# Performance work log

Hardware: AMD Instinct MI355X
Metric: run time of the kernel (lower is better)

## Reference

```python
import jax, jax.numpy as jnp
import numpy as np

B, S, D = 2, 2048, 2048
H, G = 32, 8           # num_heads, num_groups
HD = D // H            # head_dim = 64
GS = H // G            # group_size = 4


def setup_inputs() -> dict:
    key = jax.random.key(0)
    ks = jax.random.split(key, 11)
    s = 0.02
    return {
        "x": jax.random.normal(ks[0], (B, S, D), dtype=jnp.float32),
        "kv": jax.random.normal(ks[1], (B, S, D), dtype=jnp.float32),
        "Wq": jax.random.normal(ks[2], (D, D), dtype=jnp.float32) * s,
        "bq": jnp.zeros((D,), dtype=jnp.float32),
        "Wk": jax.random.normal(ks[3], (D, G * HD), dtype=jnp.float32) * s,
        "bk": jnp.zeros((G * HD,), dtype=jnp.float32),
        "Wv": jax.random.normal(ks[4], (D, G * HD), dtype=jnp.float32) * s,
        "bv": jnp.zeros((G * HD,), dtype=jnp.float32),
        "Wo": jax.random.normal(ks[5], (D, D), dtype=jnp.float32) * s,
        "bo": jnp.zeros((D,), dtype=jnp.float32),
        "expanding_context": 0,
    }


def reference(x, kv, Wq, bq, Wk, bk, Wv, bv, Wo, bo, expanding_context):
    # expanding_context is ignored when use_kv_cache=False (matches torch module)
    b, s, d = x.shape
    q = (x @ Wq + bq).reshape(b, s, H, HD).transpose(0, 2, 1, 3)      # [B,H,S,HD]
    k = (kv @ Wk + bk).reshape(b, s, G, HD).transpose(0, 2, 1, 3)     # [B,G,S,HD]
    v = (kv @ Wv + bv).reshape(b, s, G, HD).transpose(0, 2, 1, 3)     # [B,G,S,HD]
    # repeat_interleave KV heads to match query heads
    k = jnp.repeat(k, GS, axis=1)                                      # [B,H,S,HD]
    v = jnp.repeat(v, GS, axis=1)
    scale = 1.0 / jnp.sqrt(jnp.array(HD, dtype=x.dtype))
    scores = jnp.einsum("bhqd,bhkd->bhqk", q, k) * scale              # [B,H,S,S]
    causal = jnp.tril(jnp.ones((s, s), dtype=bool))                    # True where allowed
    scores = jnp.where(causal[None, None], scores, jnp.finfo(x.dtype).min)
    attn = jax.nn.softmax(scores, axis=-1)
    out = jnp.einsum("bhqk,bhkd->bhqd", attn, v)                      # [B,H,S,HD]
    out = out.transpose(0, 2, 1, 3).reshape(b, s, D)                  # [B,S,D]
    return out @ Wo + bo
```

## Files before the change

kernel.cpp:

```cpp
#include <hip/hip_runtime.h>
#include <hip/hip_bf16.h>
#include <stdint.h>

namespace {
constexpr int CB = 2, CS = 2048, CD = 2048, CH = 32, CG = 8, CHD = 64, CGS = 4;

typedef __bf16 bf16x8 __attribute__((ext_vector_type(8)));
typedef float f32x4 __attribute__((ext_vector_type(4)));
typedef float f32x16 __attribute__((ext_vector_type(16)));
typedef uint32_t u32x4 __attribute__((ext_vector_type(4)));

__device__ inline uint16_t f2bf(float f) {
  uint32_t u = __float_as_uint(f);
  u += 0x7fffu + ((u >> 16) & 1u);
  return (uint16_t)(u >> 16);
}

__device__ inline void gload_lds16(const void* g, void* l) {
  __builtin_amdgcn_global_load_lds(
      (const __attribute__((address_space(1))) void*)g,
      (__attribute__((address_space(3))) void*)l, 16, 0, 0);
}

__device__ inline uint32_t cvtpk_bf16(float lo, float hi) {
  uint32_t r;
  asm("v_cvt_pk_bf16_f32 %0, %1, %2" : "=v"(r) : "v"(lo), "v"(hi));
  return r;
}
__device__ inline void pl32swap(uint32_t& a, uint32_t& b) {
  asm("v_permlane32_swap_b32 %0, %1" : "+v"(a), "+v"(b));
}
}

__global__ __launch_bounds__(256) void cast_both_kernel(
    const float* __restrict__ x, const float* __restrict__ kv,
    uint16_t* __restrict__ xb, uint16_t* __restrict__ kvb, int nel) {
  int i = (blockIdx.x * 256 + threadIdx.x) * 4;
  const float* in;
  uint16_t* out;
  if (i < nel) { in = x + i; out = xb + i; }
  else         { in = kv + (i - nel); out = kvb + (i - nel); }
  const float4 v = *(const float4*)in;
  ushort4 o;
  o.x = f2bf(v.x); o.y = f2bf(v.y); o.z = f2bf(v.z); o.w = f2bf(v.w);
  *(ushort4*)out = o;
}

__global__ __launch_bounds__(256) void transpose_all_kernel(
    const float* __restrict__ Wq, const float* __restrict__ Wk,
    const float* __restrict__ Wv, const float* __restrict__ Wo,
    uint16_t* __restrict__ out) {
  __shared__ uint16_t tile[32][33];
  const int gn0 = blockIdx.x * 32;
  const int k0 = blockIdx.y * 32;
  const float* in;
  int Nr, start;
  if (gn0 < 2048)      { in = Wq; Nr = 2048; start = 0; }
  else if (gn0 < 2560) { in = Wk; Nr = 512;  start = 2048; }
  else if (gn0 < 3072) { in = Wv; Nr = 512;  start = 2560; }
  else                 { in = Wo; Nr = 2048; start = 3072; }
  const int n0 = gn0 - start;
  const int tx = threadIdx.x & 31, tg = threadIdx.x >> 5;
#pragma unroll
  for (int rr = 0; rr < 4; ++rr) {
    int k = tg * 4 + rr;
    tile[k][tx] = f2bf(in[(size_t)(k0 + k) * Nr + n0 + tx]);
  }
  __syncthreads();
#pragma unroll
  for (int rr = 0; rr < 4; ++rr) {
    int n = tg * 4 + rr;
    out[(size_t)(gn0 + n) * CD + k0 + tx] = tile[tx][n];
  }
}

__global__ __launch_bounds__(512, 2) void gemm_qkv_kernel(
    const uint16_t* __restrict__ xb, const uint16_t* __restrict__ kvb,
    const uint16_t* __restrict__ WT,
    const float* __restrict__ bq, const float* __restrict__ bk,
    const float* __restrict__ bv,
    uint16_t* __restrict__ Qb, uint16_t* __restrict__ Kb,
    uint16_t* __restrict__ VTb) {
  constexpr int BM = 256, BN = 256, BK = 64, K = 2048;
  __shared__ uint16_t Asm[2][BM * BK];
  __shared__ uint16_t Bsm[2][BN * BK];
  const int tid = threadIdx.x;
  const int w = tid >> 6, l = tid & 63;
  const int wr = w >> 2, wc = w & 3;
  const int l15 = l & 15, lq = l >> 4;

  const int gx = gridDim.x;
  int bid = blockIdx.y * gx + blockIdx.x;
  const int nwg = gx * gridDim.y;
  bid = (bid & 7) * (nwg >> 3) + (bid >> 3);
  const int m0 = (bid / gx) * BM, n0 = (bid % gx) * BN;
  const uint16_t* A = (n0 < 2048) ? xb : kvb;

  auto stage = [&](int buf, int kt) {
#pragma unroll
    for (int i = 0; i < 4; ++i) {
      int g = i * 512 + tid;
      int row = g >> 3, slot = g & 7;
      int kq = slot ^ (row & 7);
      gload_lds16(A + (size_t)(m0 + row) * K + kt + kq * 8, &Asm[buf][g * 8]);
    }
#pragma unroll
    for (int i = 0; i < 4; ++i) {
      int g = i * 512 + tid;
      int row = g >> 3, slot = g & 7;
      int kq = slot ^ (row & 7);
      gload_lds16(WT + (size_t)(n0 + row) * K + kt + kq * 8, &Bsm[buf][g * 8]);
    }
  };

  f32x4 acc[8][4] = {};

  stage(0, 0);
  asm volatile("s_waitcnt vmcnt(0)" ::: "memory");
  __syncthreads();
  int cur = 0;

  for (int kt = 0; kt < K; kt += BK) {
    if (kt + BK < K) stage(cur ^ 1, kt + BK);

    const char* Ab = (const char*)&Asm[cur][0];
    const char* Bb = (const char*)&Bsm[cur][0];
#pragma unroll
    for (int kk = 0; kk < 2; ++kk) {
      bf16x8 af[8], bfr[4];
#pragma unroll
      for (int m = 0; m < 8; ++m) {
        int row = wr * 128 + m * 16 + l15;
        int boff = ((row * BK + kk * 32 + lq * 8) * 2) ^ ((row & 7) << 4);
        af[m] = *(const bf16x8*)(Ab + boff);
      }
#pragma unroll
      for (int n = 0; n < 4; ++n) {
        int row = wc * 64 + n * 16 + l15;
        int boff = ((row * BK + kk * 32 + lq * 8) * 2) ^ ((row & 7) << 4);
        bfr[n] = *(const bf16x8*)(Bb + boff);
      }
#pragma unroll
      for (int m = 0; m < 8; ++m)
#pragma unroll
        for (int n = 0; n < 4; ++n)
          acc[m][n] = __builtin_amdgcn_mfma_f32_16x16x32_bf16(
              af[m], bfr[n], acc[m][n], 0, 0, 0);
    }

    asm volatile("s_waitcnt vmcnt(0)" ::: "memory");
    __syncthreads();
    cur ^= 1;
  }

#pragma unroll
  for (int m = 0; m < 8; ++m)
#pragma unroll
    for (int n = 0; n < 4; ++n)
#pragma unroll
      for (int r = 0; r < 4; ++r) {
        int gm = m0 + wr * 128 + m * 16 + lq * 4 + r;
        int gn = n0 + wc * 64 + n * 16 + l15;
        int b = gm >> 11, s = gm & (CS - 1);
        if (n0 < 2048) {
          float v = (acc[m][n][r] + bq[gn]) * (0.125f * 1.44269504088896340736f);
          int h = gn >> 6, hd = gn & 63;
          Qb[(((size_t)(b * CH + h)) * CS + s) * CHD + hd] = f2bf(v);
        } else if (n0 < 2560) {
          int gn2 = gn - 2048;
          float v = acc[m][n][r] + bk[gn2];
          int gh = gn2 >> 6, hd = gn2 & 63;
          Kb[(((size_t)(b * CG + gh)) * CS + s) * CHD + hd] = f2bf(v);
        } else {
          int gn2 = gn - 2560;
          float v = acc[m][n][r] + bv[gn2];
          int gh = gn2 >> 6, hd = gn2 & 63;
          VTb[(((size_t)(b * CG + gh)) * CHD + hd) * CS + s] = f2bf(v);
        }
      }
}

__global__ __launch_bounds__(512, 2) void gemm_out_kernel(
    const uint16_t* __restrict__ A, const uint16_t* __restrict__ Bt,
    const float* __restrict__ bias, float* __restrict__ Cout,
    int M, int N, int K) {
  constexpr int BM = 256, BN = 128, BK = 64;
  __shared__ uint16_t Asm[2][BM * BK];
  __shared__ uint16_t Bsm[2][BN * BK];
  const int tid = threadIdx.x;
  const int w = tid >> 6, l = tid & 63;
  const int wr = w >> 2, wc = w & 3;
  const int l15 = l & 15, lq = l >> 4;

  const int gx = gridDim.x;
  int bid = blockIdx.y * gx + blockIdx.x;
  const int nwg = gx * gridDim.y;
  bid = (bid & 7) * (nwg >> 3) + (bid >> 3);
  const int m0 = (bid / gx) * BM, n0 = (bid % gx) * BN;

  auto stage = [&](int buf, int kt) {
#pragma unroll
    for (int i = 0; i < 4; ++i) {
      int g = i * 512 + tid;
      int row = g >> 3, slot = g & 7;
      int kq = slot ^ (row & 7);
      gload_lds16(A + (size_t)(m0 + row) * K + kt + kq * 8, &Asm[buf][g * 8]);
    }
#pragma unroll
    for (int i = 0; i < 2; ++i) {
      int g = i * 512 + tid;
      int row = g >> 3, slot = g & 7;
      int kq = slot ^ (row & 7);
      gload_lds16(Bt + (size_t)(n0 + row) * K + kt + kq * 8, &Bsm[buf][g * 8]);
    }
  };

  f32x4 acc[8][2] = {};

  stage(0, 0);
  asm volatile("s_waitcnt vmcnt(0)" ::: "memory");
  __syncthreads();
  int cur = 0;

  for (int kt = 0; kt < K; kt += BK) {
    if (kt + BK < K) stage(cur ^ 1, kt + BK);

    const char* Ab = (const char*)&Asm[cur][0];
    const char* Bb = (const char*)&Bsm[cur][0];
#pragma unroll
    for (int kk = 0; kk < 2; ++kk) {
      bf16x8 af[8], bfr[2];
#pragma unroll
      for (int m = 0; m < 8; ++m) {
        int row = wr * 128 + m * 16 + l15;
        int boff = ((row * BK + kk * 32 + lq * 8) * 2) ^ ((row & 7) << 4);
        af[m] = *(const bf16x8*)(Ab + boff);
      }
#pragma unroll
      for (int n = 0; n < 2; ++n) {
        int row = wc * 32 + n * 16 + l15;
        int boff = ((row * BK + kk * 32 + lq * 8) * 2) ^ ((row & 7) << 4);
        bfr[n] = *(const bf16x8*)(Bb + boff);
      }
#pragma unroll
      for (int m = 0; m < 8; ++m)
#pragma unroll
        for (int n = 0; n < 2; ++n)
          acc[m][n] = __builtin_amdgcn_mfma_f32_16x16x32_bf16(
              af[m], bfr[n], acc[m][n], 0, 0, 0);
    }

    asm volatile("s_waitcnt vmcnt(0)" ::: "memory");
    __syncthreads();
    cur ^= 1;
  }

#pragma unroll
  for (int m = 0; m < 8; ++m)
#pragma unroll
    for (int n = 0; n < 2; ++n)
#pragma unroll
      for (int r = 0; r < 4; ++r) {
        int gm = m0 + wr * 128 + m * 16 + lq * 4 + r;
        int gn = n0 + wc * 32 + n * 16 + l15;
        Cout[(size_t)gm * N + gn] = acc[m][n][r] + bias[gn];
      }
}

__global__ __launch_bounds__(256) void flash_attn_kernel(
    const uint16_t* __restrict__ Q, const uint16_t* __restrict__ K,
    const uint16_t* __restrict__ VT, uint16_t* __restrict__ Aout) {
  constexpr int NQB = CS / 128;
  __shared__ __align__(16) uint16_t Ksm[2][64 * 64];
  __shared__ __align__(16) uint16_t Vsm[2][64 * 64];
  const int tid = threadIdx.x, w = tid >> 6, l = tid & 63;
  const int l31 = l & 31, hi = l >> 5;
  const int x = blockIdx.x;
  const int h = blockIdx.y, b = blockIdx.z, g = h >> 2;

  const uint16_t* Qbase = Q + ((size_t)(b * CH + h)) * CS * CHD;
  const uint16_t* Kbase = K + ((size_t)(b * CG + g)) * CS * CHD;
  const uint16_t* Vbase = VT + ((size_t)(b * CG + g)) * CHD * CS;

  const int srow = tid >> 3, sslot = tid & 7;
  const int skq = sslot ^ (srow & 7);
  const uint16_t* kSrc0 = Kbase + (size_t)srow * CHD + skq * 8;
  const uint16_t* kSrc1 = kSrc0 + 32 * CHD;
  const uint16_t* vSrc0 = Vbase + (size_t)srow * CS + skq * 8;
  const uint16_t* vSrc1 = vSrc0 + 32 * CS;
  uint16_t* kDst0 = &Ksm[0][0] + tid * 8;
  uint16_t* vDst0 = &Vsm[0][0] + tid * 8;

  int qkOff[2][4];
#pragma unroll
  for (int c = 0; c < 2; ++c)
#pragma unroll
    for (int kc = 0; kc < 4; ++kc) {
      int row = c * 32 + l31;
      qkOff[c][kc] = ((row * 64 + kc * 16 + hi * 8) * 2) ^ ((row & 7) << 4);
    }

  auto stage = [&](int buf, int kt) {
    const size_t ko = (size_t)kt * 64 * CHD;
    const int vo = kt * 64;
    uint16_t* kd = kDst0 + buf * 64 * 64;
    uint16_t* vd = vDst0 + buf * 64 * 64;
    gload_lds16(kSrc0 + ko, kd);
    gload_lds16(kSrc1 + ko, kd + 2048);
    gload_lds16(vSrc0 + vo, vd);
    gload_lds16(vSrc1 + vo, vd + 2048);
  };

#pragma unroll 1
  for (int job = 0; job < 2; ++job) {
    const int qb = job == 0 ? (NQB - 1 - x) : x;
    const int qrow = qb * 128 + w * 32 + l31;
    const int wtop = qb * 128 + w * 32 + 31;

    bf16x8 qf[4];
#pragma unroll
    for (int kc = 0; kc < 4; ++kc)
      qf[kc] = *(const bf16x8*)(Qbase + (size_t)qrow * CHD + kc * 16 + hi * 8);

    f32x16 o0 = {}, o1 = {};
    float mrun = -3e38f, lrun = 0.f;
    const int nt = 2 * qb + 2;

    stage(0, 0);
    asm volatile("s_waitcnt vmcnt(0)" ::: "memory");
    __syncthreads();

    for (int kt = 0; kt < nt; ++kt) {
      const int cur = kt & 1;
      if (kt + 1 < nt) stage(cur ^ 1, kt + 1);

      if (kt * 64 <= wtop) {
        const char* ksmb = (const char*)Ksm[cur];
        const char* vsmb = (const char*)Vsm[cur];

        f32x16 p0 = {}, p1 = {};
        __builtin_amdgcn_s_setprio(1);
#pragma unroll
        for (int kc = 0; kc < 4; ++kc) {
          bf16x8 ka0 = *(const bf16x8*)(ksmb + qkOff[0][kc]);
          bf16x8 ka1 = *(const bf16x8*)(ksmb + qkOff[1][kc]);
          p0 = __builtin_amdgcn_mfma_f32_32x32x16_bf16(ka0, qf[kc], p0, 0, 0, 0);
          p1 = __builtin_amdgcn_mfma_f32_32x32x16_bf16(ka1, qf[kc], p1, 0, 0, 0);
        }
        __builtin_amdgcn_s_setprio(0);

        const bool need_mask = (kt * 64 + 63 > qb * 128 + w * 32);
        float pmax = -3e38f;
        if (need_mask) {
#pragma unroll
          for (int r = 0; r < 16; ++r) {
            int keyb = kt * 64 + (r & 3) + 8 * (r >> 2) + 4 * hi;
            if (keyb > qrow) p0[r] = -3e38f;
            if (keyb + 32 > qrow) p1[r] = -3e38f;
          }
        }
#pragma unroll
        for (int r = 0; r < 16; ++r) {
          pmax = fmaxf(pmax, p0[r]);
          pmax = fmaxf(pmax, p1[r]);
        }
        pmax = fmaxf(pmax, __shfl_xor(pmax, 32));

        if (!__all(pmax <= mrun + 8.f)) {
          float mnew = fmaxf(mrun, pmax);
          float alpha = __builtin_amdgcn_exp2f(mrun - mnew);
#pragma unroll
          for (int r = 0; r < 16; ++r) { o0[r] *= alpha; o1[r] *= alpha; }
          lrun *= alpha;
          mrun = mnew;
        }
        float s = 0.f;
#pragma unroll
        for (int r = 0; r < 16; ++r) {
          float e0 = __builtin_amdgcn_exp2f(p0[r] - mrun);
          float e1 = __builtin_amdgcn_exp2f(p1[r] - mrun);
          p0[r] = e0; p1[r] = e1;
          s += e0 + e1;
        }
        s += __shfl_xor(s, 32);
        lrun += s;

        u32x4 paw[4];
#pragma unroll
        for (int k = 0; k < 4; ++k) {
          const int base = (k & 1) * 8;
          const f32x16& pc = (k >> 1) ? p1 : p0;
          uint32_t c01 = cvtpk_bf16(pc[base + 0], pc[base + 1]);
          uint32_t c23 = cvtpk_bf16(pc[base + 2], pc[base + 3]);
          uint32_t c45 = cvtpk_bf16(pc[base + 4], pc[base + 5]);
          uint32_t c67 = cvtpk_bf16(pc[base + 6], pc[base + 7]);
          pl32swap(c01, c45);
          pl32swap(c23, c67);
          paw[k] = (u32x4){c01, c23, c45, c67};
        }

        __builtin_amdgcn_s_setprio(1);
#pragma unroll
        for (int ks = 0; ks < 4; ++ks) {
          bf16x8 vb0 = *(const bf16x8*)(vsmb + qkOff[0][ks]);
          bf16x8 vb1 = *(const bf16x8*)(vsmb + qkOff[1][ks]);
          bf16x8 pb = __builtin_bit_cast(bf16x8, paw[ks]);
          o0 = __builtin_amdgcn_mfma_f32_32x32x16_bf16(vb0, pb, o0, 0, 0, 0);
          o1 = __builtin_amdgcn_mfma_f32_32x32x16_bf16(vb1, pb, o1, 0, 0, 0);
        }
        __builtin_amdgcn_s_setprio(0);
      }

      asm volatile("s_waitcnt vmcnt(0)" ::: "memory");
      __syncthreads();
    }

    float invl = 1.f / lrun;
    uint16_t* orow = Aout + ((size_t)b * CS + qrow) * CD + (size_t)h * CHD;
#pragma unroll
    for (int k = 0; k < 8; ++k) {
      int reg = 2 * k;
      int hd = (reg & 3) + 8 * (reg >> 2) + 4 * hi;
      *(uint32_t*)(orow + hd) = cvtpk_bf16(o0[reg] * invl, o0[reg + 1] * invl);
      *(uint32_t*)(orow + hd + 32) = cvtpk_bf16(o1[reg] * invl, o1[reg + 1] * invl);
    }
  }
}

extern "C" void kernel_launch(void* const* d_in, const int* in_sizes, int n_in,
                              void* d_out, int out_size, void* d_ws, size_t ws_size,
                              hipStream_t stream) {
  const float* x = (const float*)d_in[0];
  const float* kv = (const float*)d_in[1];
  const float* Wq = (const float*)d_in[2];
  const float* bq = (const float*)d_in[3];
  const float* Wk = (const float*)d_in[4];
  const float* bk = (const float*)d_in[5];
  const float* Wv = (const float*)d_in[6];
  const float* bv = (const float*)d_in[7];
  const float* Wo = (const float*)d_in[8];
  const float* bo = (const float*)d_in[9];
  float* out = (float*)d_out;

  char* ws = (char*)d_ws;
  uint16_t* xb = (uint16_t*)ws;   ws += (size_t)CB * CS * CD * 2;
  uint16_t* kvb = (uint16_t*)ws;  ws += (size_t)CB * CS * CD * 2;
  uint16_t* WqT = (uint16_t*)ws;  ws += (size_t)CD * CD * 2;
  uint16_t* WkT = (uint16_t*)ws;  ws += (size_t)(CG * CHD) * CD * 2;
  uint16_t* WvT = (uint16_t*)ws;  ws += (size_t)(CG * CHD) * CD * 2;
  uint16_t* WoT = (uint16_t*)ws;  ws += (size_t)CD * CD * 2;
  uint16_t* Qb = (uint16_t*)ws;   ws += (size_t)CB * CH * CS * CHD * 2;
  uint16_t* Kb = (uint16_t*)ws;   ws += (size_t)CB * CG * CS * CHD * 2;
  uint16_t* VTb = (uint16_t*)ws;  ws += (size_t)CB * CG * CHD * CS * 2;
  uint16_t* attnb = (uint16_t*)ws;
  (void)WkT; (void)WvT;

  const int NTOK = CB * CS;
  const int nel = CB * CS * CD;

  cast_both_kernel<<<2 * nel / 4 / 256, 256, 0, stream>>>(x, kv, xb, kvb, nel);
  transpose_all_kernel<<<dim3(5120 / 32, CD / 32), 256, 0, stream>>>(
      Wq, Wk, Wv, Wo, WqT);

  gemm_qkv_kernel<<<dim3(3072 / 256, NTOK / 256), 512, 0, stream>>>(
      xb, kvb, WqT, bq, bk, bv, Qb, Kb, VTb);

  flash_attn_kernel<<<dim3(CS / 256, CH, CB), 256, 0, stream>>>(Qb, Kb, VTb, attnb);

  gemm_out_kernel<<<dim3(CD / 128, NTOK / 256), 512, 0, stream>>>(
      attnb, WoT, bo, out, NTOK, CD, CD);
}
```

Measured before the change: 232.3 us.

## Triple-buffer GEMM K-tiles with BK=32 and single barrier per step

Both projection GEMMs move from a double-buffered BK=64 loop with two barriers per step to a three-stage ring of BK=32 tiles. Each step waits on a partial vmcnt, issues one barrier, reads fragments, then prefetches two tiles ahead before running the MFMAs at raised wave priority. LDS offsets are precomputed and the swizzle changes to a 4-slot XOR. The aim is to hide global-load latency and cut barrier stalls, at the cost of twice as many loop iterations. The out GEMM now hardcodes K=2048 and ignores its K argument, and the vmcnt counts must match the number of loads each stage issues.

```diff
diff --git a/kernel.cpp b/kernel.cpp
--- a/kernel.cpp
+++ b/kernel.cpp
@@ -81,9 +81,11 @@
     const float* __restrict__ bv,
     uint16_t* __restrict__ Qb, uint16_t* __restrict__ Kb,
     uint16_t* __restrict__ VTb) {
-  constexpr int BM = 256, BN = 256, BK = 64, K = 2048;
-  __shared__ uint16_t Asm[2][BM * BK];
-  __shared__ uint16_t Bsm[2][BN * BK];
+  constexpr int BM = 256, BN = 256, BK = 32, K = 2048, NT = K / BK;
+  constexpr int ASZ = BM * BK;
+  constexpr int BSZ = BN * BK;
+  constexpr int BUFSZ = ASZ + BSZ;
+  __shared__ uint16_t smem[3 * BUFSZ];
   const int tid = threadIdx.x;
   const int w = tid >> 6, l = tid & 63;
   const int wr = w >> 2, wc = w & 3;
@@ -97,60 +99,69 @@
   const uint16_t* A = (n0 < 2048) ? xb : kvb;
 
   auto stage = [&](int buf, int kt) {
-#pragma unroll
-    for (int i = 0; i < 4; ++i) {
+    uint16_t* base = smem + buf * BUFSZ;
+    const int k0 = kt * BK;
+#pragma unroll
+    for (int i = 0; i < 2; ++i) {
       int g = i * 512 + tid;
-      int row = g >> 3, slot = g & 7;
-      int kq = slot ^ (row & 7);
-      gload_lds16(A + (size_t)(m0 + row) * K + kt + kq * 8, &Asm[buf][g * 8]);
-    }
-#pragma unroll
-    for (int i = 0; i < 4; ++i) {
+      int row = g >> 2, slot = g & 3;
+      int kq = slot ^ (row & 3);
+      gload_lds16(A + (size_t)(m0 + row) * K + k0 + kq * 8, base + g * 8);
+    }
+#pragma unroll
+    for (int i = 0; i < 2; ++i) {
       int g = i * 512 + tid;
-      int row = g >> 3, slot = g & 7;
-      int kq = slot ^ (row & 7);
-      gload_lds16(WT + (size_t)(n0 + row) * K + kt + kq * 8, &Bsm[buf][g * 8]);
+      int row = g >> 2, slot = g & 3;
+      int kq = slot ^ (row & 3);
+      gload_lds16(WT + (size_t)(n0 + row) * K + k0 + kq * 8,
+                  base + ASZ + g * 8);
     }
   };
 
+  int aOff[8], bOff[4];
+#pragma unroll
+  for (int m = 0; m < 8; ++m) {
+    int row = wr * 128 + m * 16 + l15;
+    aOff[m] = (row * BK + (lq ^ (row & 3)) * 8) * 2;
+  }
+#pragma unroll
+  for (int n = 0; n < 4; ++n) {
+    int row = wc * 64 + n * 16 + l15;
+    bOff[n] = ASZ * 2 + (row * BK + (lq ^ (row & 3)) * 8) * 2;
+  }
+
   f32x4 acc[8][4] = {};
 
   stage(0, 0);
-  asm volatile("s_waitcnt vmcnt(0)" ::: "memory");
-  __syncthreads();
-  int cur = 0;
-
-  for (int kt = 0; kt < K; kt += BK) {
-    if (kt + BK < K) stage(cur ^ 1, kt + BK);
-
-    const char* Ab = (const char*)&Asm[cur][0];
-    const char* Bb = (const char*)&Bsm[cur][0];
-#pragma unroll
-    for (int kk = 0; kk < 2; ++kk) {
-      bf16x8 af[8], bfr[4];
-#pragma unroll
-      for (int m = 0; m < 8; ++m) {
-        int row = wr * 128 + m * 16 + l15;
-        int boff = ((row * BK + kk * 32 + lq * 8) * 2) ^ ((row & 7) << 4);
-        af[m] = *(const bf16x8*)(Ab + boff);
-      }
-#pragma unroll
-      for (int n = 0; n < 4; ++n) {
-        int row = wc * 64 + n * 16 + l15;
-        int boff = ((row * BK + kk * 32 + lq * 8) * 2) ^ ((row & 7) << 4);
-        bfr[n] = *(const bf16x8*)(Bb + boff);
-      }
-#pragma unroll
-      for (int m = 0; m < 8; ++m)
-#pragma unroll
-        for (int n = 0; n < 4; ++n)
-          acc[m][n] = __builtin_amdgcn_mfma_f32_16x16x32_bf16(
-              af[m], bfr[n], acc[m][n], 0, 0, 0);
-    }
-
-    asm volatile("s_waitcnt vmcnt(0)" ::: "memory");
-    __syncthreads();
-    cur ^= 1;
+  stage(1, 1);
+
+  int bt = 0, bs = 2;
+  for (int t = 0; t < NT; ++t) {
+    if (t < NT - 1) asm volatile("s_waitcnt vmcnt(4)" ::: "memory");
+    else            asm volatile("s_waitcnt vmcnt(0)" ::: "memory");
+    __builtin_amdgcn_s_barrier();
+    asm volatile("" ::: "memory");
+
+    const char* buf = (const char*)(smem + bt * BUFSZ);
+    bf16x8 af[8], bfr[4];
+#pragma unroll
+    for (int m = 0; m < 8; ++m) af[m] = *(const bf16x8*)(buf + aOff[m]);
+#pragma unroll
+    for (int n = 0; n < 4; ++n) bfr[n] = *(const bf16x8*)(buf + bOff[n]);
+
+    if (t + 2 < NT) stage(bs, t + 2);
+
+    __builtin_amdgcn_s_setprio(1);
+#pragma unroll
+    for (int m = 0; m < 8; ++m)
+#pragma unroll
+      for (int n = 0; n < 4; ++n)
+        acc[m][n] = __builtin_amdgcn_mfma_f32_16x16x32_bf16(
+            af[m], bfr[n], acc[m][n], 0, 0, 0);
+    __builtin_amdgcn_s_setprio(0);
+
+    bt = bt == 2 ? 0 : bt + 1;
+    bs = bs == 2 ? 0 : bs + 1;
   }
 
 #pragma unroll
@@ -183,10 +194,12 @@
 __global__ __launch_bounds__(512, 2) void gemm_out_kernel(
     const uint16_t* __restrict__ A, const uint16_t* __restrict__ Bt,
     const float* __restrict__ bias, float* __restrict__ Cout,
-    int M, int N, int K) {
-  constexpr int BM = 256, BN = 128, BK = 64;
-  __shared__ uint16_t Asm[2][BM * BK];
-  __shared__ uint16_t Bsm[2][BN * BK];
+    int M, int N, int Kdim) {
+  constexpr int BM = 256, BN = 128, BK = 32, K = 2048, NT = K / BK;
+  constexpr int ASZ = BM * BK;
+  constexpr int BSZ = BN * BK;
+  constexpr int BUFSZ = ASZ + BSZ;
+  __shared__ uint16_t smem[3 * BUFSZ];
   const int tid = threadIdx.x;
   const int w = tid >> 6, l = tid & 63;
   const int wr = w >> 2, wc = w & 3;
@@ -199,60 +212,68 @@
   const int m0 = (bid / gx) * BM, n0 = (bid % gx) * BN;
 
   auto stage = [&](int buf, int kt) {
-#pragma unroll
-    for (int i = 0; i < 4; ++i) {
-      int g = i * 512 + tid;
-      int row = g >> 3, slot = g & 7;
-      int kq = slot ^ (row & 7);
-      gload_lds16(A + (size_t)(m0 + row) * K + kt + kq * 8, &Asm[buf][g * 8]);
-    }
+    uint16_t* base = smem + buf * BUFSZ;
+    const int k0 = kt * BK;
 #pragma unroll
     for (int i = 0; i < 2; ++i) {
       int g = i * 512 + tid;
-      int row = g >> 3, slot = g & 7;
-      int kq = slot ^ (row & 7);
-      gload_lds16(Bt + (size_t)(n0 + row) * K + kt + kq * 8, &Bsm[buf][g * 8]);
+      int row = g >> 2, slot = g & 3;
+      int kq = slot ^ (row & 3);
+      gload_lds16(A + (size_t)(m0 + row) * K + k0 + kq * 8, base + g * 8);
+    }
+    {
+      int g = tid;
+      int row = g >> 2, slot = g & 3;
+      int kq = slot ^ (row & 3);
+      gload_lds16(Bt + (size_t)(n0 + row) * K + k0 + kq * 8,
+                  base + ASZ + g * 8);
     }
   };
 
+  int aOff[8], bOff[2];
+#pragma unroll
+  for (int m = 0; m < 8; ++m) {
+    int row = wr * 128 + m * 16 + l15;
+    aOff[m] = (row * BK + (lq ^ (row & 3)) * 8) * 2;
+  }
+#pragma unroll
+  for (int n = 0; n < 2; ++n) {
+    int row = wc * 32 + n * 16 + l15;
+    bOff[n] = ASZ * 2 + (row * BK + (lq ^ (row & 3)) * 8) * 2;
+  }
+
   f32x4 acc[8][2] = {};
 
   stage(0, 0);
-  asm volatile("s_waitcnt vmcnt(0)" ::: "memory");
-  __syncthreads();
-  int cur = 0;
-
-  for (int kt = 0; kt < K; kt += BK) {
-    if (kt + BK < K) stage(cur ^ 1, kt + BK);
-
-    const char* Ab = (const char*)&Asm[cur][0];
-    const char* Bb = (const char*)&Bsm[cur][0];
-#pragma unroll
-    for (int kk = 0; kk < 2; ++kk) {
-      bf16x8 af[8], bfr[2];
-#pragma unroll
-      for (int m = 0; m < 8; ++m) {
-        int row = wr * 128 + m * 16 + l15;
-        int boff = ((row * BK + kk * 32 + lq * 8) * 2) ^ ((row & 7) << 4);
-        af[m] = *(const bf16x8*)(Ab + boff);
-      }
-#pragma unroll
-      for (int n = 0; n < 2; ++n) {
-        int row = wc * 32 + n * 16 + l15;
-        int boff = ((row * BK + kk * 32 + lq * 8) * 2) ^ ((row & 7) << 4);
-        bfr[n] = *(const bf16x8*)(Bb + boff);
-      }
-#pragma unroll
-      for (int m = 0; m < 8; ++m)
-#pragma unroll
-        for (int n = 0; n < 2; ++n)
-          acc[m][n] = __builtin_amdgcn_mfma_f32_16x16x32_bf16(
-              af[m], bfr[n], acc[m][n], 0, 0, 0);
-    }
-
-    asm volatile("s_waitcnt vmcnt(0)" ::: "memory");
-    __syncthreads();
-    cur ^= 1;
+  stage(1, 1);
+
+  int bt = 0, bs = 2;
+  for (int t = 0; t < NT; ++t) {
+    if (t < NT - 1) asm volatile("s_waitcnt vmcnt(3)" ::: "memory");
+    else            asm volatile("s_waitcnt vmcnt(0)" ::: "memory");
+    __builtin_amdgcn_s_barrier();
+    asm volatile("" ::: "memory");
+
+    const char* buf = (const char*)(smem + bt * BUFSZ);
+    bf16x8 af[8], bfr[2];
+#pragma unroll
+    for (int m = 0; m < 8; ++m) af[m] = *(const bf16x8*)(buf + aOff[m]);
+#pragma unroll
+    for (int n = 0; n < 2; ++n) bfr[n] = *(const bf16x8*)(buf + bOff[n]);
+
+    if (t + 2 < NT) stage(bs, t + 2);
+
+    __builtin_amdgcn_s_setprio(1);
+#pragma unroll
+    for (int m = 0; m < 8; ++m)
+#pragma unroll
+      for (int n = 0; n < 2; ++n)
+        acc[m][n] = __builtin_amdgcn_mfma_f32_16x16x32_bf16(
+            af[m], bfr[n], acc[m][n], 0, 0, 0);
+    __builtin_amdgcn_s_setprio(0);
+
+    bt = bt == 2 ? 0 : bt + 1;
+    bs = bs == 2 ? 0 : bs + 1;
   }
 
 #pragma unroll
```

New measurement: 217.6 us. 1.07x faster.
